# Optimization experiments

Measured on AMD Instinct MI355X. Metric: run time of the kernel, lower is better.

Reference implementation:

```python
import jax, jax.numpy as jnp
import numpy as np

B, T, I, H = 128, 512, 256, 512  # batch, seq_len, num_encoder_tokens, latent_dim


def setup_inputs() -> dict:
    key = jax.random.key(0)
    k0, k1, k2, k3, k4 = jax.random.split(key, 5)
    s = 1.0 / np.sqrt(H).astype(np.float32)  # PyTorch GRU init: U(-1/sqrt(H), 1/sqrt(H))
    return {
        "encoder_inputs": jax.random.normal(k0, (B, T, I), dtype=jnp.float32),
        "W_ih": jax.random.uniform(k1, (3 * H, I), jnp.float32, -s, s),
        "W_hh": jax.random.uniform(k2, (3 * H, H), jnp.float32, -s, s),
        "b_ih": jax.random.uniform(k3, (3 * H,), jnp.float32, -s, s),
        "b_hh": jax.random.uniform(k4, (3 * H,), jnp.float32, -s, s),
    }


def _gru_final_state(encoder_inputs, W_ih, W_hh, b_ih, b_hh):
    # Precompute input projections for all timesteps in one big GEMM: [B,T,3H]
    x_gates = jnp.einsum('bti,gi->btg', encoder_inputs, W_ih) + b_ih
    x_gates = jnp.swapaxes(x_gates, 0, 1)  # [T,B,3H] for scan over time
    Hdim = W_hh.shape[1]
    h0 = jnp.zeros((encoder_inputs.shape[0], Hdim), encoder_inputs.dtype)

    def step(h, xg):
        hg = h @ W_hh.T + b_hh                      # [B,3H]
        xr, xz, xn = jnp.split(xg, 3, axis=-1)      # PyTorch gate order: r, z, n
        hr, hz, hn = jnp.split(hg, 3, axis=-1)
        r = jax.nn.sigmoid(xr + hr)
        z = jax.nn.sigmoid(xz + hz)
        n = jnp.tanh(xn + r * hn)
        h_new = (1.0 - z) * n + z * h
        return h_new, None

    h_final, _ = jax.lax.scan(step, h0, x_gates)
    return h_final[None]  # [num_layers=1, B, H], matching torch's state_h


def reference(encoder_inputs, W_ih, W_hh, b_ih, b_hh):
    return _gru_final_state(encoder_inputs, W_ih, W_hh, b_ih, b_hh)
```

## Files before the change

### kernel.cpp

```cpp
#include <hip/hip_runtime.h>
#include <hip/hip_bf16.h>

#define BB   128
#define TT   512
#define II   256
#define HH   512
#define G3   1536

typedef __attribute__((ext_vector_type(8))) short short8;
typedef __attribute__((ext_vector_type(4))) float f32x4;

__device__ __forceinline__ float bf2f(unsigned short u) {
    union { unsigned int u; float f; } p; p.u = ((unsigned int)u) << 16; return p.f;
}
__device__ __forceinline__ unsigned short f2bf(float f) {
    union { float f; unsigned int u; } p; p.f = f;
    unsigned int r = p.u + 0x7fffu + ((p.u >> 16) & 1u);
    return (unsigned short)(r >> 16);
}
__device__ __forceinline__ float sigmoidf_fast(float x) {
    return 1.0f / (1.0f + __expf(-x));
}
__device__ __forceinline__ float tanhf_fast(float x) {
    return 1.0f - 2.0f / (1.0f + __expf(2.0f * x));
}

__global__ __launch_bounds__(256) void xgate_gemm(
    const float* __restrict__ x,
    const float* __restrict__ Wih,
    const float* __restrict__ bih,
    unsigned short* __restrict__ xg)
{
    __shared__ unsigned short AS[128][40];
    __shared__ unsigned short BS[128][40];

    const int t   = blockIdx.y;
    const int g0  = blockIdx.x * 128;
    const int tid = threadIdx.x;
    const int lane = tid & 63;
    const int w    = tid >> 6;
    const int wr   = w >> 1, wc = w & 1;

    f32x4 acc[4][4];
#pragma unroll
    for (int a = 0; a < 4; ++a)
#pragma unroll
        for (int b = 0; b < 4; ++b) acc[a][b] = (f32x4)(0.0f);

    for (int kk = 0; kk < 8; ++kk) {
        const int k0 = kk * 32;
#pragma unroll
        for (int ii = 0; ii < 4; ++ii) {
            int slot = tid + 256 * ii;
            int row  = slot >> 3;
            int c4   = slot & 7;
            float4 av = *(const float4*)(x + ((size_t)row * TT + t) * II + k0 + c4 * 4);
            unsigned short* ap = &AS[row][c4 * 4];
            ap[0] = f2bf(av.x); ap[1] = f2bf(av.y); ap[2] = f2bf(av.z); ap[3] = f2bf(av.w);
            float4 bv = *(const float4*)(Wih + (size_t)(g0 + row) * II + k0 + c4 * 4);
            unsigned short* bp = &BS[row][c4 * 4];
            bp[0] = f2bf(bv.x); bp[1] = f2bf(bv.y); bp[2] = f2bf(bv.z); bp[3] = f2bf(bv.w);
        }
        __syncthreads();

        const int kc = (lane >> 4) * 8;
        short8 a[4], b[4];
#pragma unroll
        for (int mi = 0; mi < 4; ++mi)
            a[mi] = *(const short8*)&AS[wr * 64 + mi * 16 + (lane & 15)][kc];
#pragma unroll
        for (int ni = 0; ni < 4; ++ni)
            b[ni] = *(const short8*)&BS[wc * 64 + ni * 16 + (lane & 15)][kc];
#pragma unroll
        for (int mi = 0; mi < 4; ++mi)
#pragma unroll
            for (int ni = 0; ni < 4; ++ni)
                acc[mi][ni] = __builtin_amdgcn_mfma_f32_16x16x32_bf16(a[mi], b[ni], acc[mi][ni], 0, 0, 0);
        __syncthreads();
    }

#pragma unroll
    for (int ni = 0; ni < 4; ++ni) {
        const int col = wc * 64 + ni * 16 + (lane & 15);
        const float bias = bih[g0 + col];
#pragma unroll
        for (int mi = 0; mi < 4; ++mi) {
#pragma unroll
            for (int i = 0; i < 4; ++i) {
                const int row = wr * 64 + mi * 16 + (lane >> 4) * 4 + i;
                xg[((size_t)t * BB + row) * G3 + g0 + col] = f2bf(acc[mi][ni][i] + bias);
            }
        }
    }
}

#define NTH2 128

__global__ __launch_bounds__(NTH2, 1) void gru_scan(
    const unsigned short* __restrict__ xg,
    const float* __restrict__ Whh,
    const float* __restrict__ bhh,
    float* __restrict__ out,
    unsigned long long* __restrict__ hb64)
{
    __shared__ unsigned int hF[4096];

    const int g    = blockIdx.x & 7;
    const int m    = blockIdx.x >> 3;
    const int tid  = threadIdx.x;
    const int lane = tid & 63;
    const int w    = tid >> 6;

    short8 Wr[3][16];
    {
        const int jrow = m * 32 + w * 16 + (lane & 15);
        const int kofs = (lane >> 4) * 8;
#pragma unroll
        for (int q = 0; q < 3; ++q) {
            const float* wrow = Whh + ((size_t)(q * HH + jrow)) * HH + kofs;
#pragma unroll
            for (int ks = 0; ks < 16; ++ks) {
                float4 v0 = *(const float4*)(wrow + ks * 32);
                float4 v1 = *(const float4*)(wrow + ks * 32 + 4);
                union { short8 s; unsigned int u[4]; } pk;
                pk.u[0] = (unsigned int)f2bf(v0.x) | ((unsigned int)f2bf(v0.y) << 16);
                pk.u[1] = (unsigned int)f2bf(v0.z) | ((unsigned int)f2bf(v0.w) << 16);
                pk.u[2] = (unsigned int)f2bf(v1.x) | ((unsigned int)f2bf(v1.y) << 16);
                pk.u[3] = (unsigned int)f2bf(v1.z) | ((unsigned int)f2bf(v1.w) << 16);
                Wr[q][ks] = pk.s;
            }
        }
    }

    const int jj = m * 32 + w * 16 + (lane & 15);
    const float bhr = bhh[jj];
    const float bhz = bhh[HH + jj];
    const float bhn = bhh[2 * HH + jj];
    const int b0 = (lane >> 4) * 4;

    float hh[4] = {0.0f, 0.0f, 0.0f, 0.0f};

    const unsigned char* hA = (const unsigned char*)hF + lane * 16;

    for (int t = 0; t < TT; ++t) {
        const unsigned short* xp = xg + ((size_t)t * BB + g * 16) * G3 + jj;
        float xr[4], xz[4], xn[4];
#pragma unroll
        for (int i = 0; i < 4; ++i) {
            const unsigned short* p = xp + (size_t)(b0 + i) * G3;
            xr[i] = bf2f(p[0]); xz[i] = bf2f(p[HH]); xn[i] = bf2f(p[2 * HH]);
        }

        const unsigned long long want = (unsigned long long)t;
        const unsigned long long* src = hb64 + ((size_t)(t & 1) * BB + (size_t)g * 16) * 256;
        unsigned long long v[32];
        while (true) {
            bool ok = true;
#pragma unroll
            for (int i = 0; i < 32; ++i) {
                int widx = i * NTH2 + tid;
                int e2 = widx & 3, row = (widx >> 2) & 15;
                int lg = (widx >> 6) & 3, ks = (widx >> 8) & 15;
                int pair = ks * 16 + lg * 4 + e2;
                v[i] = __hip_atomic_load(&src[(size_t)row * 256 + pair],
                                         __ATOMIC_RELAXED, __HIP_MEMORY_SCOPE_AGENT);
                ok &= ((v[i] >> 32) == want);
            }
            if (ok) break;
        }
#pragma unroll
        for (int i = 0; i < 32; ++i) {
            int widx = i * NTH2 + tid;
            int e2 = widx & 3, row = (widx >> 2) & 15;
            int lg = (widx >> 6) & 3, ks = (widx >> 8) & 15;
            hF[ks * 256 + lg * 64 + row * 4 + e2] = (unsigned int)v[i];
        }
        __syncthreads();

        f32x4 aR = (f32x4)(0.0f), aZ = (f32x4)(0.0f), aN = (f32x4)(0.0f);
#pragma unroll
        for (int ks = 0; ks < 16; ++ks) {
            short8 a = *(const short8*)(hA + ks * 1024);
            aR = __builtin_amdgcn_mfma_f32_16x16x32_bf16(a, Wr[0][ks], aR, 0, 0, 0);
            aZ = __builtin_amdgcn_mfma_f32_16x16x32_bf16(a, Wr[1][ks], aZ, 0, 0, 0);
            aN = __builtin_amdgcn_mfma_f32_16x16x32_bf16(a, Wr[2][ks], aN, 0, 0, 0);
        }
        __syncthreads();

        const unsigned long long tag = ((unsigned long long)(t + 1)) << 32;
        unsigned long long* dst = hb64 + (size_t)((t + 1) & 1) * BB * 256;
#pragma unroll
        for (int i = 0; i < 4; ++i) {
            float r = sigmoidf_fast(xr[i] + aR[i] + bhr);
            float z = sigmoidf_fast(xz[i] + aZ[i] + bhz);
            float n = tanhf_fast(xn[i] + r * (aN[i] + bhn));
            hh[i] = (1.0f - z) * n + z * hh[i];
            unsigned int u  = (unsigned int)f2bf(hh[i]);
            unsigned int pv = (unsigned int)__shfl_xor((int)u, 1);
            if ((lane & 1) == 0) {
                unsigned long long word = tag | (unsigned long long)(u | (pv << 16));
                __hip_atomic_store(&dst[(size_t)(g * 16 + b0 + i) * 256 + (jj >> 1)], word,
                                   __ATOMIC_RELAXED, __HIP_MEMORY_SCOPE_AGENT);
            }
            if (t == TT - 1)
                out[(size_t)(g * 16 + b0 + i) * HH + jj] = hh[i];
        }
    }
}

extern "C" void kernel_launch(void* const* d_in, const int* in_sizes, int n_in,
                              void* d_out, int out_size, void* d_ws, size_t ws_size,
                              hipStream_t stream) {
    const float* x   = (const float*)d_in[0];
    const float* Wih = (const float*)d_in[1];
    const float* Whh = (const float*)d_in[2];
    const float* bih = (const float*)d_in[3];
    const float* bhh = (const float*)d_in[4];
    float* out = (float*)d_out;

    const size_t XG_BYTES   = (size_t)TT * BB * G3 * 2;
    unsigned short* xg      = (unsigned short*)d_ws;
    unsigned long long* hb64 = (unsigned long long*)((char*)d_ws + XG_BYTES);
    const size_t HBUF_BYTES = (size_t)2 * BB * 256 * 8;

    hipMemsetAsync((char*)d_ws + XG_BYTES, 0, HBUF_BYTES, stream);

    dim3 g1(G3 / 128, TT);
    xgate_gemm<<<g1, 256, 0, stream>>>(x, Wih, bih, xg);

    gru_scan<<<128, NTH2, 0, stream>>>(xg, Whh, bhh, out, hb64);
}
```

Measured before the change: 1.839 ms.

## Use single-wave scan blocks reading tagged hidden state directly into MFMA operands

The recurrent scan kernel now runs 256 single-wavefront blocks instead of 128 two-wave blocks, each owning 16 hidden columns. Each lane polls the tagged hidden-state buffer with 16-byte cache-bypassing loads laid out to match its MFMA A-operand fragment, retrying only the chunks whose tags are stale. This removes the LDS staging and both block barriers on the per-timestep critical path. In exchange, each block issues more global traffic per step and twice as many blocks take part in the cross-block handshake.

```diff
diff --git a/kernel.cpp b/kernel.cpp
--- a/kernel.cpp
+++ b/kernel.cpp
@@ -9,6 +9,7 @@
 
 typedef __attribute__((ext_vector_type(8))) short short8;
 typedef __attribute__((ext_vector_type(4))) float f32x4;
+typedef __attribute__((ext_vector_type(4))) unsigned int u32x4;
 
 __device__ __forceinline__ float bf2f(unsigned short u) {
     union { unsigned int u; float f; } p; p.u = ((unsigned int)u) << 16; return p.f;
@@ -23,6 +24,11 @@
 }
 __device__ __forceinline__ float tanhf_fast(float x) {
     return 1.0f - 2.0f / (1.0f + __expf(2.0f * x));
+}
+
+__device__ __forceinline__ void gld16(u32x4& dst, const void* addr) {
+    asm volatile("global_load_dwordx4 %0, %1, off sc0 sc1"
+                 : "=v"(dst) : "v"(addr));
 }
 
 __global__ __launch_bounds__(256) void xgate_gemm(
@@ -94,30 +100,24 @@
     }
 }
 
-#define NTH2 128
-
-__global__ __launch_bounds__(NTH2, 1) void gru_scan(
+__global__ __launch_bounds__(64, 1) void gru_scan(
     const unsigned short* __restrict__ xg,
     const float* __restrict__ Whh,
     const float* __restrict__ bhh,
     float* __restrict__ out,
     unsigned long long* __restrict__ hb64)
 {
-    __shared__ unsigned int hF[4096];
-
     const int g    = blockIdx.x & 7;
-    const int m    = blockIdx.x >> 3;
-    const int tid  = threadIdx.x;
-    const int lane = tid & 63;
-    const int w    = tid >> 6;
-
+    const int mm   = blockIdx.x >> 3;
+    const int lane = threadIdx.x & 63;
+
+    const int jj = mm * 16 + (lane & 15);
     short8 Wr[3][16];
     {
-        const int jrow = m * 32 + w * 16 + (lane & 15);
         const int kofs = (lane >> 4) * 8;
 #pragma unroll
         for (int q = 0; q < 3; ++q) {
-            const float* wrow = Whh + ((size_t)(q * HH + jrow)) * HH + kofs;
+            const float* wrow = Whh + ((size_t)(q * HH + jj)) * HH + kofs;
 #pragma unroll
             for (int ks = 0; ks < 16; ++ks) {
                 float4 v0 = *(const float4*)(wrow + ks * 32);
@@ -132,7 +132,6 @@
         }
     }
 
-    const int jj = m * 32 + w * 16 + (lane & 15);
     const float bhr = bhh[jj];
     const float bhz = bhh[HH + jj];
     const float bhn = bhh[2 * HH + jj];
@@ -140,7 +139,9 @@
 
     float hh[4] = {0.0f, 0.0f, 0.0f, 0.0f};
 
-    const unsigned char* hA = (const unsigned char*)hF + lane * 16;
+    const char* rowb0 = (const char*)hb64 +
+        (((size_t)g * 16 + (lane & 15)) * 256 + ((lane >> 4) << 2)) * 8;
+    const size_t PARITY_B = (size_t)BB * 256 * 8;
 
     for (int t = 0; t < TT; ++t) {
         const unsigned short* xp = xg + ((size_t)t * BB + g * 16) * G3 + jj;
@@ -151,41 +152,43 @@
             xr[i] = bf2f(p[0]); xz[i] = bf2f(p[HH]); xn[i] = bf2f(p[2 * HH]);
         }
 
-        const unsigned long long want = (unsigned long long)t;
-        const unsigned long long* src = hb64 + ((size_t)(t & 1) * BB + (size_t)g * 16) * 256;
-        unsigned long long v[32];
+        const unsigned int want = (unsigned int)t;
+        const char* pb = rowb0 + (size_t)(t & 1) * PARITY_B;
+        u32x4 d2[32];
+        unsigned int done = 0;
         while (true) {
-            bool ok = true;
-#pragma unroll
-            for (int i = 0; i < 32; ++i) {
-                int widx = i * NTH2 + tid;
-                int e2 = widx & 3, row = (widx >> 2) & 15;
-                int lg = (widx >> 6) & 3, ks = (widx >> 8) & 15;
-                int pair = ks * 16 + lg * 4 + e2;
-                v[i] = __hip_atomic_load(&src[(size_t)row * 256 + pair],
-                                         __ATOMIC_RELAXED, __HIP_MEMORY_SCOPE_AGENT);
-                ok &= ((v[i] >> 32) == want);
-            }
-            if (ok) break;
-        }
-#pragma unroll
-        for (int i = 0; i < 32; ++i) {
-            int widx = i * NTH2 + tid;
-            int e2 = widx & 3, row = (widx >> 2) & 15;
-            int lg = (widx >> 6) & 3, ks = (widx >> 8) & 15;
-            hF[ks * 256 + lg * 64 + row * 4 + e2] = (unsigned int)v[i];
-        }
-        __syncthreads();
+#pragma unroll
+            for (int ks = 0; ks < 16; ++ks) {
+                if (!(done & (1u << ks))) {
+                    gld16(d2[2 * ks],     pb + ks * 128);
+                    gld16(d2[2 * ks + 1], pb + ks * 128 + 16);
+                }
+            }
+            asm volatile("s_waitcnt vmcnt(0)" ::: "memory");
+            __builtin_amdgcn_sched_barrier(0);
+#pragma unroll
+            for (int ks = 0; ks < 16; ++ks) {
+                if (!(done & (1u << ks))) {
+                    if (d2[2 * ks][1] == want && d2[2 * ks][3] == want &&
+                        d2[2 * ks + 1][1] == want && d2[2 * ks + 1][3] == want)
+                        done |= 1u << ks;
+                }
+            }
+            if (__all(done == 0xffffu)) break;
+        }
 
         f32x4 aR = (f32x4)(0.0f), aZ = (f32x4)(0.0f), aN = (f32x4)(0.0f);
 #pragma unroll
         for (int ks = 0; ks < 16; ++ks) {
-            short8 a = *(const short8*)(hA + ks * 1024);
-            aR = __builtin_amdgcn_mfma_f32_16x16x32_bf16(a, Wr[0][ks], aR, 0, 0, 0);
-            aZ = __builtin_amdgcn_mfma_f32_16x16x32_bf16(a, Wr[1][ks], aZ, 0, 0, 0);
-            aN = __builtin_amdgcn_mfma_f32_16x16x32_bf16(a, Wr[2][ks], aN, 0, 0, 0);
-        }
-        __syncthreads();
+            union { short8 s; unsigned int u[4]; } pk;
+            pk.u[0] = d2[2 * ks][0];
+            pk.u[1] = d2[2 * ks][2];
+            pk.u[2] = d2[2 * ks + 1][0];
+            pk.u[3] = d2[2 * ks + 1][2];
+            aR = __builtin_amdgcn_mfma_f32_16x16x32_bf16(pk.s, Wr[0][ks], aR, 0, 0, 0);
+            aZ = __builtin_amdgcn_mfma_f32_16x16x32_bf16(pk.s, Wr[1][ks], aZ, 0, 0, 0);
+            aN = __builtin_amdgcn_mfma_f32_16x16x32_bf16(pk.s, Wr[2][ks], aN, 0, 0, 0);
+        }
 
         const unsigned long long tag = ((unsigned long long)(t + 1)) << 32;
         unsigned long long* dst = hb64 + (size_t)((t + 1) & 1) * BB * 256;
@@ -228,5 +231,5 @@
     dim3 g1(G3 / 128, TT);
     xgate_gemm<<<g1, 256, 0, stream>>>(x, Wih, bih, xg);
 
-    gru_scan<<<128, NTH2, 0, stream>>>(xg, Whh, bhh, out, hb64);
-}
+    gru_scan<<<256, 64, 0, stream>>>(xg, Whh, bhh, out, hb64);
+}
```

Measured after the change: 2.732 ms. 48.5% more time.

## Vectorize h polling, double-buffer LDS, prefetch next-step x gates

Applied to the files above, without the earlier changes.

The recurrent scan kernel now polls the shared hidden-state buffer with 16 wide dwordx4 loads per thread (cache-bypassing sc0 sc1) instead of 32 separate 64-bit atomic loads, and checks the tags in bulk. The LDS staging buffer for h is double-buffered by timestep parity, so the second __syncthreads per step can be dropped. The input-gate values for step t+1 are loaded while step t runs, keeping global reads off the critical path, and the final output store moves out of the loop. The inline asm that skips compiler-visible atomics relies on the per-address tag check for correctness, and the larger LDS footprint and extra registers could affect scheduling.

```diff
diff --git a/kernel.cpp b/kernel.cpp
--- a/kernel.cpp
+++ b/kernel.cpp
@@ -9,6 +9,7 @@
 
 typedef __attribute__((ext_vector_type(8))) short short8;
 typedef __attribute__((ext_vector_type(4))) float f32x4;
+typedef __attribute__((ext_vector_type(4))) unsigned int u32x4;
 
 __device__ __forceinline__ float bf2f(unsigned short u) {
     union { unsigned int u; float f; } p; p.u = ((unsigned int)u) << 16; return p.f;
@@ -24,6 +25,10 @@
 __device__ __forceinline__ float tanhf_fast(float x) {
     return 1.0f - 2.0f / (1.0f + __expf(2.0f * x));
 }
+
+#define GLD16O(dst, base, OFFSTR)                                         \
+    asm volatile("global_load_dwordx4 %0, %1, off offset:" OFFSTR " sc0 sc1" \
+                 : "=v"(dst) : "v"(base))
 
 __global__ __launch_bounds__(256) void xgate_gemm(
     const float* __restrict__ x,
@@ -103,7 +108,7 @@
     float* __restrict__ out,
     unsigned long long* __restrict__ hb64)
 {
-    __shared__ unsigned int hF[4096];
+    __shared__ unsigned int hF[2 * 4096];
 
     const int g    = blockIdx.x & 7;
     const int m    = blockIdx.x >> 3;
@@ -111,13 +116,13 @@
     const int lane = tid & 63;
     const int w    = tid >> 6;
 
+    const int jj = m * 32 + w * 16 + (lane & 15);
     short8 Wr[3][16];
     {
-        const int jrow = m * 32 + w * 16 + (lane & 15);
         const int kofs = (lane >> 4) * 8;
 #pragma unroll
         for (int q = 0; q < 3; ++q) {
-            const float* wrow = Whh + ((size_t)(q * HH + jrow)) * HH + kofs;
+            const float* wrow = Whh + ((size_t)(q * HH + jj)) * HH + kofs;
 #pragma unroll
             for (int ks = 0; ks < 16; ++ks) {
                 float4 v0 = *(const float4*)(wrow + ks * 32);
@@ -132,7 +137,6 @@
         }
     }
 
-    const int jj = m * 32 + w * 16 + (lane & 15);
     const float bhr = bhh[jj];
     const float bhz = bhh[HH + jj];
     const float bhn = bhh[2 * HH + jj];
@@ -140,43 +144,68 @@
 
     float hh[4] = {0.0f, 0.0f, 0.0f, 0.0f};
 
-    const unsigned char* hA = (const unsigned char*)hF + lane * 16;
+    const int prow = tid & 15;
+    const int plg  = (tid >> 4) & 3;
+    const int pe2  = tid >> 6;
+    const char* pollb = (const char*)hb64 +
+        (((size_t)g * 16 + prow) * 256 + plg * 4 + pe2 * 2) * 8;
+    const size_t PARITY_B = (size_t)BB * 256 * 8;
+    const int dstb = plg * 64 + prow * 4 + pe2 * 2;
+
+    const unsigned int* xg32 = (const unsigned int*)xg;
+    const unsigned int xsel = (unsigned int)(jj & 1) * 16;
+    unsigned int xoff[12];
+#pragma unroll
+    for (int i = 0; i < 4; ++i)
+#pragma unroll
+        for (int q = 0; q < 3; ++q)
+            xoff[i * 3 + q] = (unsigned int)(((g * 16 + b0 + i) * G3 + q * HH + (jj & ~1)) >> 1);
+    const unsigned int XSTEP = (unsigned int)((BB * G3) >> 1);
+
+    unsigned int xc[12];
+#pragma unroll
+    for (int v = 0; v < 12; ++v) xc[v] = xg32[xoff[v]];
 
     for (int t = 0; t < TT; ++t) {
-        const unsigned short* xp = xg + ((size_t)t * BB + g * 16) * G3 + jj;
-        float xr[4], xz[4], xn[4];
-#pragma unroll
-        for (int i = 0; i < 4; ++i) {
-            const unsigned short* p = xp + (size_t)(b0 + i) * G3;
-            xr[i] = bf2f(p[0]); xz[i] = bf2f(p[HH]); xn[i] = bf2f(p[2 * HH]);
-        }
-
-        const unsigned long long want = (unsigned long long)t;
-        const unsigned long long* src = hb64 + ((size_t)(t & 1) * BB + (size_t)g * 16) * 256;
-        unsigned long long v[32];
+        const unsigned int want = (unsigned int)t;
+        const char* pb = pollb + (size_t)(t & 1) * PARITY_B;
+        u32x4 P[16];
         while (true) {
+            GLD16O(P[ 0], pb, "0");    GLD16O(P[ 1], pb, "128");
+            GLD16O(P[ 2], pb, "256");  GLD16O(P[ 3], pb, "384");
+            GLD16O(P[ 4], pb, "512");  GLD16O(P[ 5], pb, "640");
+            GLD16O(P[ 6], pb, "768");  GLD16O(P[ 7], pb, "896");
+            GLD16O(P[ 8], pb, "1024"); GLD16O(P[ 9], pb, "1152");
+            GLD16O(P[10], pb, "1280"); GLD16O(P[11], pb, "1408");
+            GLD16O(P[12], pb, "1536"); GLD16O(P[13], pb, "1664");
+            GLD16O(P[14], pb, "1792"); GLD16O(P[15], pb, "1920");
+            asm volatile("s_waitcnt vmcnt(0)" ::: "memory");
+            __builtin_amdgcn_sched_barrier(0);
             bool ok = true;
 #pragma unroll
-            for (int i = 0; i < 32; ++i) {
-                int widx = i * NTH2 + tid;
-                int e2 = widx & 3, row = (widx >> 2) & 15;
-                int lg = (widx >> 6) & 3, ks = (widx >> 8) & 15;
-                int pair = ks * 16 + lg * 4 + e2;
-                v[i] = __hip_atomic_load(&src[(size_t)row * 256 + pair],
-                                         __ATOMIC_RELAXED, __HIP_MEMORY_SCOPE_AGENT);
-                ok &= ((v[i] >> 32) == want);
-            }
+            for (int ks = 0; ks < 16; ++ks)
+                ok &= (P[ks][1] == want) & (P[ks][3] == want);
             if (ok) break;
         }
-#pragma unroll
-        for (int i = 0; i < 32; ++i) {
-            int widx = i * NTH2 + tid;
-            int e2 = widx & 3, row = (widx >> 2) & 15;
-            int lg = (widx >> 6) & 3, ks = (widx >> 8) & 15;
-            hF[ks * 256 + lg * 64 + row * 4 + e2] = (unsigned int)v[i];
-        }
+
+        unsigned int* hD = &hF[(t & 1) * 4096 + dstb];
+#pragma unroll
+        for (int ks = 0; ks < 16; ++ks) {
+            unsigned long long dv = (unsigned long long)P[ks][0] |
+                                    ((unsigned long long)P[ks][2] << 32);
+            *(unsigned long long*)&hD[ks * 256] = dv;
+        }
+
+        unsigned int xn[12];
+        {
+            const unsigned int tw = (t < TT - 1 ? (unsigned int)(t + 1) : (unsigned int)t) * XSTEP;
+#pragma unroll
+            for (int v = 0; v < 12; ++v) xn[v] = xg32[xoff[v] + tw];
+        }
+
         __syncthreads();
 
+        const char* hA = (const char*)hF + (t & 1) * 16384 + lane * 16;
         f32x4 aR = (f32x4)(0.0f), aZ = (f32x4)(0.0f), aN = (f32x4)(0.0f);
 #pragma unroll
         for (int ks = 0; ks < 16; ++ks) {
@@ -185,15 +214,17 @@
             aZ = __builtin_amdgcn_mfma_f32_16x16x32_bf16(a, Wr[1][ks], aZ, 0, 0, 0);
             aN = __builtin_amdgcn_mfma_f32_16x16x32_bf16(a, Wr[2][ks], aN, 0, 0, 0);
         }
-        __syncthreads();
 
         const unsigned long long tag = ((unsigned long long)(t + 1)) << 32;
         unsigned long long* dst = hb64 + (size_t)((t + 1) & 1) * BB * 256;
 #pragma unroll
         for (int i = 0; i < 4; ++i) {
-            float r = sigmoidf_fast(xr[i] + aR[i] + bhr);
-            float z = sigmoidf_fast(xz[i] + aZ[i] + bhz);
-            float n = tanhf_fast(xn[i] + r * (aN[i] + bhn));
+            float xr = bf2f((unsigned short)(xc[i * 3 + 0] >> xsel));
+            float xz = bf2f((unsigned short)(xc[i * 3 + 1] >> xsel));
+            float xn_ = bf2f((unsigned short)(xc[i * 3 + 2] >> xsel));
+            float r = sigmoidf_fast(xr + aR[i] + bhr);
+            float z = sigmoidf_fast(xz + aZ[i] + bhz);
+            float n = tanhf_fast(xn_ + r * (aN[i] + bhn));
             hh[i] = (1.0f - z) * n + z * hh[i];
             unsigned int u  = (unsigned int)f2bf(hh[i]);
             unsigned int pv = (unsigned int)__shfl_xor((int)u, 1);
@@ -202,10 +233,15 @@
                 __hip_atomic_store(&dst[(size_t)(g * 16 + b0 + i) * 256 + (jj >> 1)], word,
                                    __ATOMIC_RELAXED, __HIP_MEMORY_SCOPE_AGENT);
             }
-            if (t == TT - 1)
-                out[(size_t)(g * 16 + b0 + i) * HH + jj] = hh[i];
-        }
-    }
+        }
+
+#pragma unroll
+        for (int v = 0; v < 12; ++v) xc[v] = xn[v];
+    }
+
+#pragma unroll
+    for (int i = 0; i < 4; ++i)
+        out[(size_t)(g * 16 + b0 + i) * HH + jj] = hh[i];
 }
 
 extern "C" void kernel_launch(void* const* d_in, const int* in_sizes, int n_in,
```

Measured after the change: 1.820 ms. Within noise of the previous version (-1.0%).
